# Optimization experiments

Hardware: AMD Instinct MI355X
Metric: run time of the kernel (lower is better)

Reference implementation:

```python
import jax, jax.numpy as jnp
import numpy as np

B, N, I, O, R = 8, 1024, 256, 256, 8


def setup_inputs() -> dict:
    key = jax.random.key(0)
    k1, k2, k3 = jax.random.split(key, 3)
    x = jax.random.normal(k1, (B, N, I), dtype=jnp.float32)
    adj = jax.random.uniform(k2, (B, N, N, R), dtype=jnp.float32)  # soft adjacency [b, src, dst, r]
    weight = jax.random.normal(k3, (R, I, O), dtype=jnp.float32)   # per-relation transform
    return {"x": x, "adj": adj, "weight": weight}


def reference(x, adj, weight):
    # per-relation transformed features: [b, src, r, o]
    f = jnp.einsum('bni,rio->bnro', x, weight)
    # contraction over source nodes and relations, weighted by soft adjacency:
    # out[b, dst, o] = sum_{src, r} adj[b, src, dst, r] * f[b, src, r, o]
    out = jnp.einsum('bnro,bnmr->bmo', f, adj)
    # normalization: total incoming soft-edge weight per destination node
    denom = jnp.clip(adj.sum(axis=(1, 3)), 1e-16, None)  # [b, dst]
    return out / denom[..., None]
```

## Files before the change

### kernel.cpp

```cpp
#include <hip/hip_runtime.h>
#include <stdint.h>


typedef float          floatx4  __attribute__((ext_vector_type(4)));
typedef short          shortx8  __attribute__((ext_vector_type(8)));
typedef unsigned short ushortx4 __attribute__((ext_vector_type(4)));
typedef unsigned short ushortx8 __attribute__((ext_vector_type(8)));

__device__ __forceinline__ unsigned short f2bf(float f) {
  union { float f; unsigned int u; } v; v.f = f;
  unsigned int u = v.u + 0x7FFFu + ((v.u >> 16) & 1u);
  return (unsigned short)(u >> 16);
}

__device__ __forceinline__ void gload16(const void* g, void* l) {
  __builtin_amdgcn_global_load_lds((__attribute__((address_space(1))) void*)g,
                                   (__attribute__((address_space(3))) void*)l,
                                   16, 0, 0);
}

__global__ __launch_bounds__(256) void prep_xw(const float* __restrict__ x,
                                               const float* __restrict__ w,
                                               unsigned short* __restrict__ xbf,
                                               unsigned short* __restrict__ wt) {
  int bid = blockIdx.x;
  if (bid < 1024) {
    int t = bid * 256 + threadIdx.x;
    const float4* p = (const float4*)x + (size_t)t * 2;
    float4 a = p[0], b4 = p[1];
    ushortx8 o;
    o[0] = f2bf(a.x);  o[1] = f2bf(a.y);  o[2] = f2bf(a.z);  o[3] = f2bf(a.w);
    o[4] = f2bf(b4.x); o[5] = f2bf(b4.y); o[6] = f2bf(b4.z); o[7] = f2bf(b4.w);
    *(ushortx8*)(xbf + (size_t)t * 8) = o;
  } else {
    int id = (bid - 1024) * 256 + threadIdx.x;
    int r = id >> 16, i = (id >> 8) & 255, o = id & 255;
    float v = w[((size_t)(r * 256 + i) << 8) + o];
    wt[((size_t)(o * 8 + r) << 8) + i] = f2bf(v);
  }
}

__global__ __launch_bounds__(256) void k1_gemm(const unsigned short* __restrict__ xbf,
                                               const unsigned short* __restrict__ wt,
                                               unsigned short* __restrict__ ft) {
  int bid = blockIdx.x;
  int m0 = (bid >> 4) * 128, n0 = (bid & 15) * 128;
  int l = threadIdx.x & 63, w = threadIdx.x >> 6;
  int lr = l & 15, lg = l >> 4;
  int mw = m0 + (w >> 1) * 64, nw = n0 + (w & 1) * 64;

  floatx4 acc[4][4] = {};
#pragma unroll
  for (int ks = 0; ks < 8; ++ks) {
    shortx8 a[4], b[4];
#pragma unroll
    for (int mi = 0; mi < 4; ++mi)
      a[mi] = *(const shortx8*)(xbf + (size_t)(mw + mi * 16 + lr) * 256 + ks * 32 + lg * 8);
#pragma unroll
    for (int ni = 0; ni < 4; ++ni)
      b[ni] = *(const shortx8*)(wt + (size_t)(nw + ni * 16 + lr) * 256 + ks * 32 + lg * 8);
#pragma unroll
    for (int mi = 0; mi < 4; ++mi)
#pragma unroll
      for (int ni = 0; ni < 4; ++ni)
        acc[mi][ni] = __builtin_amdgcn_mfma_f32_16x16x32_bf16(a[mi], b[ni], acc[mi][ni], 0, 0, 0);
  }
#pragma unroll
  for (int mi = 0; mi < 4; ++mi) {
#pragma unroll
    for (int ni = 0; ni < 4; ++ni) {
      int np = nw + ni * 16 + lr;
      int o = np >> 3, r = np & 7;
#pragma unroll
      for (int reg = 0; reg < 4; ++reg) {
        int row = mw + mi * 16 + lg * 4 + reg;
        int b8 = row >> 10, src = row & 1023;
        ft[((size_t)(b8 * 256 + o) << 13) + src * 8 + r] = f2bf(acc[mi][ni][reg]);
      }
    }
  }
}

#define BHALF 16384
#define AHALF 4096
__global__ __launch_bounds__(512) void k2_gemm(const float* __restrict__ adj,
                                               const unsigned short* __restrict__ ft,
                                               float* __restrict__ pout,
                                               float* __restrict__ dpart) {
  __shared__ __align__(16) unsigned short Blds[2 * BHALF];
  __shared__ __align__(16) unsigned short Alds[2 * AHALF];
  __shared__ float dsums[512];
  __shared__ float denr[64];

  int bid = blockIdx.x;
  int kc = bid >> 7;
  int inner = bid & 127;
  int b = inner & 7;
  int dst0 = (inner >> 3) * 64;

  int t = threadIdx.x, l = t & 63, w = t >> 6;
  int lr = l & 15, lg = l >> 4;
  int wm = w >> 2, wo = w & 3;

  int dst_l = (t >> 1) & 63;
  int rh = (t & 1) * 4;
  int sA = t >> 7;

  int csw = (l & 7) ^ (l >> 3);

  const size_t adj_b = (size_t)b << 23;
  const unsigned short* ftb = ft + ((size_t)b << 21);
  int src_base = kc * 512;
  const int KT = 64;

  float dsum = 0.f;
  floatx4 acc[2][4] = {};
  float4 av[2];

  auto A_load = [&](int kt, float4* v) {
#pragma unroll
    for (int j = 0; j < 2; ++j) {
      int src_l = sA + j * 4;
      v[j] = *(const float4*)(adj + adj_b + ((size_t)(src_base + kt * 8 + src_l) << 13)
                              + ((size_t)(dst0 + dst_l) << 3) + rh);
    }
  };
  auto A_store = [&](int half, const float4* v) {
#pragma unroll
    for (int j = 0; j < 2; ++j) {
      int src_l = sA + j * 4;
      float4 q = v[j];
      dsum += q.x + q.y + q.z + q.w;
      ushortx4 h;
      h[0] = f2bf(q.x); h[1] = f2bf(q.y); h[2] = f2bf(q.z); h[3] = f2bf(q.w);
      int slot = src_l ^ (dst_l & 7);
      *(ushortx4*)&Alds[half * AHALF + dst_l * 64 + slot * 8 + rh] = h;
    }
  };
  auto B_stage = [&](int kt, int half) {
    int kbase = (src_base + kt * 8) * 8;
#pragma unroll
    for (int i = 0; i < 4; ++i) {
      int orow = i * 64 + w * 8 + (l >> 3);
      const unsigned short* g = ftb + ((size_t)orow << 13) + kbase + (csw << 3);
      gload16(g, &Blds[half * BHALF + (i * 64 + w * 8) * 64]);
    }
  };
  auto compute = [&](int half) {
#pragma unroll
    for (int s = 0; s < 2; ++s) {
      int slotbase = s * 4 + lg;
      shortx8 af[2], bfr[4];
#pragma unroll
      for (int mi = 0; mi < 2; ++mi) {
        int row = wm * 32 + mi * 16 + lr;
        af[mi] = *(const shortx8*)&Alds[half * AHALF + row * 64 + ((slotbase ^ (row & 7)) << 3)];
      }
#pragma unroll
      for (int ni = 0; ni < 4; ++ni) {
        int oc = wo * 64 + ni * 16 + lr;
        bfr[ni] = *(const shortx8*)&Blds[half * BHALF + oc * 64 + ((slotbase ^ (oc & 7)) << 3)];
      }
#pragma unroll
      for (int mi = 0; mi < 2; ++mi)
#pragma unroll
        for (int ni = 0; ni < 4; ++ni)
          acc[mi][ni] = __builtin_amdgcn_mfma_f32_16x16x32_bf16(af[mi], bfr[ni], acc[mi][ni], 0, 0, 0);
    }
  };

  A_load(0, av);
  B_stage(0, 0);
  A_store(0, av);
  __syncthreads();

  for (int kt = 0; kt < KT; ++kt) {
    int cur = kt & 1, nxt = cur ^ 1;
    bool has = (kt + 1) < KT;
    if (has) A_load(kt + 1, av);
    if (has) B_stage(kt + 1, nxt);
    compute(cur);
    if (has) A_store(nxt, av);
    __syncthreads();
  }

  dsums[t] = dsum;
  __syncthreads();
  if (t < 64) {
    float s = 0.f;
#pragma unroll
    for (int sh = 0; sh < 4; ++sh) {
      s += dsums[sh * 128 + t * 2];
      s += dsums[sh * 128 + t * 2 + 1];
    }
    denr[t] = s;
  }
  __syncthreads();

#pragma unroll
  for (int mi = 0; mi < 2; ++mi) {
#pragma unroll
    for (int reg = 0; reg < 4; ++reg) {
      int row = dst0 + wm * 32 + mi * 16 + lg * 4 + reg;
#pragma unroll
      for (int ni = 0; ni < 4; ++ni) {
        int col = wo * 64 + ni * 16 + lr;
        pout[(size_t)kc * 2097152 + (((size_t)b << 10) + row) * 256 + col] = acc[mi][ni][reg];
      }
    }
  }
  if (t < 64) dpart[kc * 8192 + (b << 10) + dst0 + t] = denr[t];
}

__global__ __launch_bounds__(256) void k3_reduce(const float* __restrict__ pout,
                                                 const float* __restrict__ dpart,
                                                 float* __restrict__ outp) {
  int bid = blockIdx.x;
  size_t base = (size_t)bid * 256 + threadIdx.x;
  float v = pout[base] + pout[2097152 + base];
  float d = dpart[bid] + dpart[8192 + bid];
  outp[base] = v / fmaxf(d, 1e-16f);
}

extern "C" void kernel_launch(void* const* d_in, const int* in_sizes, int n_in,
                              void* d_out, int out_size, void* d_ws, size_t ws_size,
                              hipStream_t stream) {
  const float* x   = (const float*)d_in[0];
  const float* adj = (const float*)d_in[1];
  const float* w   = (const float*)d_in[2];
  float* out = (float*)d_out;

  char* ws = (char*)d_ws;
  unsigned short* ft  = (unsigned short*)(ws);
  unsigned short* xbf = (unsigned short*)(ws + 33554432);
  unsigned short* wt  = (unsigned short*)(ws + 37748736);
  float* pout  = (float*)(ws + 38797312);
  float* dpart = (float*)(ws + 55574528);

  prep_xw<<<3072, 256, 0, stream>>>(x, w, xbf, wt);
  k1_gemm<<<1024, 256, 0, stream>>>(xbf, wt, ft);
  k2_gemm<<<256, 512, 0, stream>>>(adj, ft, pout, dpart);
  k3_reduce<<<8192, 256, 0, stream>>>(pout, dpart, out);
}
```

Measured before the change: 149.8 us.

## Drop split-K reduction, triple-buffer k2 pipeline, vectorize k1 stores

k2_gemm now covers the full source dimension per block, with 32 destination rows instead of 64. This removes the partial-output workspace and the separate k3 reduce kernel, and normalization happens in the epilogue. The main loop uses a three-stage LDS ring, with manual vmcnt waits and raw s_barrier, so loads stay two tiles ahead. k1_gemm swaps its operand roles so each lane writes four contiguous bf16 relation values as one 8-byte store. The risks are halved MFMA work per A fragment and a longer serial K loop per block at the same grid size of 256.

```diff
diff --git a/kernel.cpp b/kernel.cpp
--- a/kernel.cpp
+++ b/kernel.cpp
@@ -18,6 +18,9 @@
                                    (__attribute__((address_space(3))) void*)l,
                                    16, 0, 0);
 }
+
+#define WAIT_V5 asm volatile("s_waitcnt vmcnt(5) lgkmcnt(0)" ::: "memory")
+#define WAIT_V0 asm volatile("s_waitcnt vmcnt(0) lgkmcnt(0)" ::: "memory")
 
 __global__ __launch_bounds__(256) void prep_xw(const float* __restrict__ x,
                                                const float* __restrict__ w,
@@ -44,182 +47,158 @@
                                                const unsigned short* __restrict__ wt,
                                                unsigned short* __restrict__ ft) {
   int bid = blockIdx.x;
-  int m0 = (bid >> 4) * 128, n0 = (bid & 15) * 128;
+  int p0 = (bid & 15) * 128, q0 = (bid >> 4) * 128;
   int l = threadIdx.x & 63, w = threadIdx.x >> 6;
   int lr = l & 15, lg = l >> 4;
-  int mw = m0 + (w >> 1) * 64, nw = n0 + (w & 1) * 64;
+  int pw = p0 + (w >> 1) * 64, qw = q0 + (w & 1) * 64;
 
   floatx4 acc[4][4] = {};
 #pragma unroll
   for (int ks = 0; ks < 8; ++ks) {
     shortx8 a[4], b[4];
 #pragma unroll
-    for (int mi = 0; mi < 4; ++mi)
-      a[mi] = *(const shortx8*)(xbf + (size_t)(mw + mi * 16 + lr) * 256 + ks * 32 + lg * 8);
-#pragma unroll
-    for (int ni = 0; ni < 4; ++ni)
-      b[ni] = *(const shortx8*)(wt + (size_t)(nw + ni * 16 + lr) * 256 + ks * 32 + lg * 8);
-#pragma unroll
-    for (int mi = 0; mi < 4; ++mi)
-#pragma unroll
-      for (int ni = 0; ni < 4; ++ni)
-        acc[mi][ni] = __builtin_amdgcn_mfma_f32_16x16x32_bf16(a[mi], b[ni], acc[mi][ni], 0, 0, 0);
-  }
-#pragma unroll
-  for (int mi = 0; mi < 4; ++mi) {
-#pragma unroll
-    for (int ni = 0; ni < 4; ++ni) {
-      int np = nw + ni * 16 + lr;
-      int o = np >> 3, r = np & 7;
-#pragma unroll
-      for (int reg = 0; reg < 4; ++reg) {
-        int row = mw + mi * 16 + lg * 4 + reg;
-        int b8 = row >> 10, src = row & 1023;
-        ft[((size_t)(b8 * 256 + o) << 13) + src * 8 + r] = f2bf(acc[mi][ni][reg]);
-      }
-    }
-  }
-}
-
-#define BHALF 16384
-#define AHALF 4096
+    for (int pi = 0; pi < 4; ++pi)
+      a[pi] = *(const shortx8*)(wt + (size_t)(pw + pi * 16 + lr) * 256 + ks * 32 + lg * 8);
+#pragma unroll
+    for (int qi = 0; qi < 4; ++qi)
+      b[qi] = *(const shortx8*)(xbf + (size_t)(qw + qi * 16 + lr) * 256 + ks * 32 + lg * 8);
+#pragma unroll
+    for (int pi = 0; pi < 4; ++pi)
+#pragma unroll
+      for (int qi = 0; qi < 4; ++qi)
+        acc[pi][qi] = __builtin_amdgcn_mfma_f32_16x16x32_bf16(a[pi], b[qi], acc[pi][qi], 0, 0, 0);
+  }
+#pragma unroll
+  for (int pi = 0; pi < 4; ++pi) {
+    int nbase = pw + pi * 16 + lg * 4;
+    int o = nbase >> 3, rb = nbase & 7;
+#pragma unroll
+    for (int qi = 0; qi < 4; ++qi) {
+      int m = qw + qi * 16 + lr;
+      int b8 = m >> 10, src = m & 1023;
+      ushortx4 h;
+      h[0] = f2bf(acc[pi][qi][0]); h[1] = f2bf(acc[pi][qi][1]);
+      h[2] = f2bf(acc[pi][qi][2]); h[3] = f2bf(acc[pi][qi][3]);
+      *(ushortx4*)(ft + ((size_t)(b8 * 256 + o) << 13) + src * 8 + rb) = h;
+    }
+  }
+}
+
+#define NKT 128
+#define BSZ (256 * 64)
+#define ASZ (32 * 64)
 __global__ __launch_bounds__(512) void k2_gemm(const float* __restrict__ adj,
                                                const unsigned short* __restrict__ ft,
-                                               float* __restrict__ pout,
-                                               float* __restrict__ dpart) {
-  __shared__ __align__(16) unsigned short Blds[2 * BHALF];
-  __shared__ __align__(16) unsigned short Alds[2 * AHALF];
+                                               float* __restrict__ outp) {
+  __shared__ __align__(16) unsigned short Blds[3 * BSZ];
+  __shared__ __align__(16) unsigned short Alds[3 * ASZ];
   __shared__ float dsums[512];
-  __shared__ float denr[64];
+  __shared__ float denr[32];
 
   int bid = blockIdx.x;
-  int kc = bid >> 7;
-  int inner = bid & 127;
-  int b = inner & 7;
-  int dst0 = (inner >> 3) * 64;
+  int b = bid & 7;
+  int dst0 = (bid >> 3) * 32;
 
   int t = threadIdx.x, l = t & 63, w = t >> 6;
   int lr = l & 15, lg = l >> 4;
   int wm = w >> 2, wo = w & 3;
 
-  int dst_l = (t >> 1) & 63;
+  int dst_l = (t >> 1) & 31;
   int rh = (t & 1) * 4;
-  int sA = t >> 7;
-
   int csw = (l & 7) ^ (l >> 3);
 
   const size_t adj_b = (size_t)b << 23;
   const unsigned short* ftb = ft + ((size_t)b << 21);
-  int src_base = kc * 512;
-  const int KT = 64;
 
   float dsum = 0.f;
-  floatx4 acc[2][4] = {};
-  float4 av[2];
-
-  auto A_load = [&](int kt, float4* v) {
-#pragma unroll
-    for (int j = 0; j < 2; ++j) {
-      int src_l = sA + j * 4;
-      v[j] = *(const float4*)(adj + adj_b + ((size_t)(src_base + kt * 8 + src_l) << 13)
-                              + ((size_t)(dst0 + dst_l) << 3) + rh);
-    }
-  };
-  auto A_store = [&](int half, const float4* v) {
-#pragma unroll
-    for (int j = 0; j < 2; ++j) {
-      int src_l = sA + j * 4;
-      float4 q = v[j];
-      dsum += q.x + q.y + q.z + q.w;
-      ushortx4 h;
-      h[0] = f2bf(q.x); h[1] = f2bf(q.y); h[2] = f2bf(q.z); h[3] = f2bf(q.w);
-      int slot = src_l ^ (dst_l & 7);
-      *(ushortx4*)&Alds[half * AHALF + dst_l * 64 + slot * 8 + rh] = h;
-    }
-  };
-  auto B_stage = [&](int kt, int half) {
-    int kbase = (src_base + kt * 8) * 8;
+  floatx4 acc[4] = {};
+  float4 av1, av2;
+
+  auto A_load = [&](int kt) -> float4 {
+    return *(const float4*)(adj + adj_b + ((size_t)(kt * 8 + w) << 13)
+                            + ((size_t)(dst0 + dst_l) << 3) + rh);
+  };
+  auto A_store = [&](float4 q, int buf) {
+    dsum += q.x + q.y + q.z + q.w;
+    ushortx4 h;
+    h[0] = f2bf(q.x); h[1] = f2bf(q.y); h[2] = f2bf(q.z); h[3] = f2bf(q.w);
+    int slot = w ^ (dst_l & 7);
+    *(ushortx4*)&Alds[buf * ASZ + dst_l * 64 + slot * 8 + rh] = h;
+  };
+  auto B_stage = [&](int kt, int buf) {
+    int kbase = kt * 64;
 #pragma unroll
     for (int i = 0; i < 4; ++i) {
       int orow = i * 64 + w * 8 + (l >> 3);
       const unsigned short* g = ftb + ((size_t)orow << 13) + kbase + (csw << 3);
-      gload16(g, &Blds[half * BHALF + (i * 64 + w * 8) * 64]);
-    }
-  };
-  auto compute = [&](int half) {
+      gload16(g, &Blds[buf * BSZ + (i * 64 + w * 8) * 64]);
+    }
+  };
+  auto compute = [&](int buf) {
 #pragma unroll
     for (int s = 0; s < 2; ++s) {
       int slotbase = s * 4 + lg;
-      shortx8 af[2], bfr[4];
-#pragma unroll
-      for (int mi = 0; mi < 2; ++mi) {
-        int row = wm * 32 + mi * 16 + lr;
-        af[mi] = *(const shortx8*)&Alds[half * AHALF + row * 64 + ((slotbase ^ (row & 7)) << 3)];
-      }
+      int arow = wm * 16 + lr;
+      shortx8 af = *(const shortx8*)&Alds[buf * ASZ + arow * 64 + ((slotbase ^ (arow & 7)) << 3)];
+      shortx8 bfr[4];
 #pragma unroll
       for (int ni = 0; ni < 4; ++ni) {
         int oc = wo * 64 + ni * 16 + lr;
-        bfr[ni] = *(const shortx8*)&Blds[half * BHALF + oc * 64 + ((slotbase ^ (oc & 7)) << 3)];
+        bfr[ni] = *(const shortx8*)&Blds[buf * BSZ + oc * 64 + ((slotbase ^ (oc & 7)) << 3)];
       }
 #pragma unroll
-      for (int mi = 0; mi < 2; ++mi)
-#pragma unroll
-        for (int ni = 0; ni < 4; ++ni)
-          acc[mi][ni] = __builtin_amdgcn_mfma_f32_16x16x32_bf16(af[mi], bfr[ni], acc[mi][ni], 0, 0, 0);
-    }
-  };
-
-  A_load(0, av);
+      for (int ni = 0; ni < 4; ++ni)
+        acc[ni] = __builtin_amdgcn_mfma_f32_16x16x32_bf16(af, bfr[ni], acc[ni], 0, 0, 0);
+    }
+  };
+
+  av1 = A_load(0);
   B_stage(0, 0);
-  A_store(0, av);
-  __syncthreads();
-
-  for (int kt = 0; kt < KT; ++kt) {
-    int cur = kt & 1, nxt = cur ^ 1;
-    bool has = (kt + 1) < KT;
-    if (has) A_load(kt + 1, av);
-    if (has) B_stage(kt + 1, nxt);
-    compute(cur);
-    if (has) A_store(nxt, av);
-    __syncthreads();
+  A_store(av1, 0);
+  av1 = A_load(1);
+  B_stage(1, 1);
+  WAIT_V5;
+  __builtin_amdgcn_s_barrier();
+
+  int c0 = 0, c1 = 1, c2 = 2;
+  for (int kt = 0; kt < NKT; ++kt) {
+    bool iss = (kt + 2) < NKT;
+    bool st  = (kt + 1) < NKT;
+    if (iss) { av2 = A_load(kt + 2); B_stage(kt + 2, c2); }
+    if (st)  { A_store(av1, c1); }
+    compute(c0);
+    if (st) {
+      if (iss) { WAIT_V5; } else { WAIT_V0; }
+      __builtin_amdgcn_s_barrier();
+    }
+    av1 = av2;
+    int tmp = c0; c0 = c1; c1 = c2; c2 = tmp;
   }
 
   dsums[t] = dsum;
   __syncthreads();
-  if (t < 64) {
+  if (t < 32) {
     float s = 0.f;
 #pragma unroll
-    for (int sh = 0; sh < 4; ++sh) {
-      s += dsums[sh * 128 + t * 2];
-      s += dsums[sh * 128 + t * 2 + 1];
+    for (int sl = 0; sl < 8; ++sl) {
+      s += dsums[sl * 64 + t * 2];
+      s += dsums[sl * 64 + t * 2 + 1];
     }
     denr[t] = s;
   }
   __syncthreads();
 
 #pragma unroll
-  for (int mi = 0; mi < 2; ++mi) {
-#pragma unroll
-    for (int reg = 0; reg < 4; ++reg) {
-      int row = dst0 + wm * 32 + mi * 16 + lg * 4 + reg;
-#pragma unroll
-      for (int ni = 0; ni < 4; ++ni) {
-        int col = wo * 64 + ni * 16 + lr;
-        pout[(size_t)kc * 2097152 + (((size_t)b << 10) + row) * 256 + col] = acc[mi][ni][reg];
-      }
-    }
-  }
-  if (t < 64) dpart[kc * 8192 + (b << 10) + dst0 + t] = denr[t];
-}
-
-__global__ __launch_bounds__(256) void k3_reduce(const float* __restrict__ pout,
-                                                 const float* __restrict__ dpart,
-                                                 float* __restrict__ outp) {
-  int bid = blockIdx.x;
-  size_t base = (size_t)bid * 256 + threadIdx.x;
-  float v = pout[base] + pout[2097152 + base];
-  float d = dpart[bid] + dpart[8192 + bid];
-  outp[base] = v / fmaxf(d, 1e-16f);
+  for (int reg = 0; reg < 4; ++reg) {
+    int rowl = wm * 16 + lg * 4 + reg;
+    float dinv = 1.f / fmaxf(denr[rowl], 1e-16f);
+    int row = dst0 + rowl;
+#pragma unroll
+    for (int ni = 0; ni < 4; ++ni) {
+      int col = wo * 64 + ni * 16 + lr;
+      outp[(((size_t)b << 10) + row) * 256 + col] = acc[ni][reg] * dinv;
+    }
+  }
 }
 
 extern "C" void kernel_launch(void* const* d_in, const int* in_sizes, int n_in,
@@ -234,11 +213,8 @@
   unsigned short* ft  = (unsigned short*)(ws);
   unsigned short* xbf = (unsigned short*)(ws + 33554432);
   unsigned short* wt  = (unsigned short*)(ws + 37748736);
-  float* pout  = (float*)(ws + 38797312);
-  float* dpart = (float*)(ws + 55574528);
 
   prep_xw<<<3072, 256, 0, stream>>>(x, w, xbf, wt);
   k1_gemm<<<1024, 256, 0, stream>>>(xbf, wt, ft);
-  k2_gemm<<<256, 512, 0, stream>>>(adj, ft, pout, dpart);
-  k3_reduce<<<8192, 256, 0, stream>>>(pout, dpart, out);
-}
+  k2_gemm<<<256, 512, 0, stream>>>(adj, ft, out);
+}
```

Result: slower. 175.4 us (+17.1%).

## Shrink k2 tiles to 32 dst rows with 256 threads; transpose k1 for vector stores

Applied to the files above, without the earlier changes.

k2 now uses 256-thread blocks, each covering 32 destination rows instead of 64, with twice as many blocks and launch bounds allowing two blocks per CU. This is meant to improve occupancy and spread the work across more CUs. The cost is that each B tile of ft is staged from global memory twice as often per destination. k1 swaps its operand roles so each lane holds four consecutive relation values and can write ft with packed 4-element bf16 stores instead of scalar scattered stores.

```diff
diff --git a/kernel.cpp b/kernel.cpp
--- a/kernel.cpp
+++ b/kernel.cpp
@@ -44,68 +44,62 @@
                                                const unsigned short* __restrict__ wt,
                                                unsigned short* __restrict__ ft) {
   int bid = blockIdx.x;
-  int m0 = (bid >> 4) * 128, n0 = (bid & 15) * 128;
+  int p0 = (bid & 15) * 128, q0 = (bid >> 4) * 128;
   int l = threadIdx.x & 63, w = threadIdx.x >> 6;
   int lr = l & 15, lg = l >> 4;
-  int mw = m0 + (w >> 1) * 64, nw = n0 + (w & 1) * 64;
+  int pw = p0 + (w >> 1) * 64, qw = q0 + (w & 1) * 64;
 
   floatx4 acc[4][4] = {};
 #pragma unroll
   for (int ks = 0; ks < 8; ++ks) {
     shortx8 a[4], b[4];
 #pragma unroll
-    for (int mi = 0; mi < 4; ++mi)
-      a[mi] = *(const shortx8*)(xbf + (size_t)(mw + mi * 16 + lr) * 256 + ks * 32 + lg * 8);
-#pragma unroll
-    for (int ni = 0; ni < 4; ++ni)
-      b[ni] = *(const shortx8*)(wt + (size_t)(nw + ni * 16 + lr) * 256 + ks * 32 + lg * 8);
-#pragma unroll
-    for (int mi = 0; mi < 4; ++mi)
-#pragma unroll
-      for (int ni = 0; ni < 4; ++ni)
-        acc[mi][ni] = __builtin_amdgcn_mfma_f32_16x16x32_bf16(a[mi], b[ni], acc[mi][ni], 0, 0, 0);
-  }
-#pragma unroll
-  for (int mi = 0; mi < 4; ++mi) {
-#pragma unroll
-    for (int ni = 0; ni < 4; ++ni) {
-      int np = nw + ni * 16 + lr;
-      int o = np >> 3, r = np & 7;
-#pragma unroll
-      for (int reg = 0; reg < 4; ++reg) {
-        int row = mw + mi * 16 + lg * 4 + reg;
-        int b8 = row >> 10, src = row & 1023;
-        ft[((size_t)(b8 * 256 + o) << 13) + src * 8 + r] = f2bf(acc[mi][ni][reg]);
-      }
-    }
-  }
-}
-
-#define BHALF 16384
-#define AHALF 4096
-__global__ __launch_bounds__(512) void k2_gemm(const float* __restrict__ adj,
-                                               const unsigned short* __restrict__ ft,
-                                               float* __restrict__ pout,
-                                               float* __restrict__ dpart) {
-  __shared__ __align__(16) unsigned short Blds[2 * BHALF];
-  __shared__ __align__(16) unsigned short Alds[2 * AHALF];
-  __shared__ float dsums[512];
-  __shared__ float denr[64];
-
-  int bid = blockIdx.x;
-  int kc = bid >> 7;
-  int inner = bid & 127;
-  int b = inner & 7;
-  int dst0 = (inner >> 3) * 64;
+    for (int pi = 0; pi < 4; ++pi)
+      a[pi] = *(const shortx8*)(wt + (size_t)(pw + pi * 16 + lr) * 256 + ks * 32 + lg * 8);
+#pragma unroll
+    for (int qi = 0; qi < 4; ++qi)
+      b[qi] = *(const shortx8*)(xbf + (size_t)(qw + qi * 16 + lr) * 256 + ks * 32 + lg * 8);
+#pragma unroll
+    for (int pi = 0; pi < 4; ++pi)
+#pragma unroll
+      for (int qi = 0; qi < 4; ++qi)
+        acc[pi][qi] = __builtin_amdgcn_mfma_f32_16x16x32_bf16(a[pi], b[qi], acc[pi][qi], 0, 0, 0);
+  }
+#pragma unroll
+  for (int pi = 0; pi < 4; ++pi) {
+    int nbase = pw + pi * 16 + lg * 4;
+    int o = nbase >> 3, rb = nbase & 7;
+#pragma unroll
+    for (int qi = 0; qi < 4; ++qi) {
+      int m = qw + qi * 16 + lr;
+      int b8 = m >> 10, src = m & 1023;
+      ushortx4 h;
+      h[0] = f2bf(acc[pi][qi][0]); h[1] = f2bf(acc[pi][qi][1]);
+      h[2] = f2bf(acc[pi][qi][2]); h[3] = f2bf(acc[pi][qi][3]);
+      *(ushortx4*)(ft + ((size_t)(b8 * 256 + o) << 13) + src * 8 + rb) = h;
+    }
+  }
+}
+
+#define BSZ (256 * 64)
+#define ASZ (32 * 64)
+__global__ __launch_bounds__(256, 2) void k2_gemm(const float* __restrict__ adj,
+                                                  const unsigned short* __restrict__ ft,
+                                                  float* __restrict__ pout,
+                                                  float* __restrict__ dpart) {
+  __shared__ __align__(16) unsigned short Blds[2 * BSZ];
+  __shared__ __align__(16) unsigned short Alds[2 * ASZ];
+
+  int bid = blockIdx.x;
+  int b = bid & 7;
+  int kc = (bid >> 3) & 1;
+  int dst0 = (bid >> 4) * 32;
 
   int t = threadIdx.x, l = t & 63, w = t >> 6;
   int lr = l & 15, lg = l >> 4;
-  int wm = w >> 2, wo = w & 3;
-
-  int dst_l = (t >> 1) & 63;
-  int rh = (t & 1) * 4;
-  int sA = t >> 7;
-
+
+  int dst_l = l >> 1;
+  int rh = (l & 1) * 4;
   int csw = (l & 7) ^ (l >> 3);
 
   const size_t adj_b = (size_t)b << 23;
@@ -120,46 +114,46 @@
   auto A_load = [&](int kt, float4* v) {
 #pragma unroll
     for (int j = 0; j < 2; ++j) {
-      int src_l = sA + j * 4;
+      int src_l = w + j * 4;
       v[j] = *(const float4*)(adj + adj_b + ((size_t)(src_base + kt * 8 + src_l) << 13)
                               + ((size_t)(dst0 + dst_l) << 3) + rh);
     }
   };
-  auto A_store = [&](int half, const float4* v) {
+  auto A_store = [&](int buf, const float4* v) {
 #pragma unroll
     for (int j = 0; j < 2; ++j) {
-      int src_l = sA + j * 4;
+      int src_l = w + j * 4;
       float4 q = v[j];
       dsum += q.x + q.y + q.z + q.w;
       ushortx4 h;
       h[0] = f2bf(q.x); h[1] = f2bf(q.y); h[2] = f2bf(q.z); h[3] = f2bf(q.w);
       int slot = src_l ^ (dst_l & 7);
-      *(ushortx4*)&Alds[half * AHALF + dst_l * 64 + slot * 8 + rh] = h;
-    }
-  };
-  auto B_stage = [&](int kt, int half) {
+      *(ushortx4*)&Alds[buf * ASZ + dst_l * 64 + slot * 8 + rh] = h;
+    }
+  };
+  auto B_stage = [&](int kt, int buf) {
     int kbase = (src_base + kt * 8) * 8;
 #pragma unroll
-    for (int i = 0; i < 4; ++i) {
-      int orow = i * 64 + w * 8 + (l >> 3);
+    for (int i = 0; i < 8; ++i) {
+      int orow = i * 32 + w * 8 + (l >> 3);
       const unsigned short* g = ftb + ((size_t)orow << 13) + kbase + (csw << 3);
-      gload16(g, &Blds[half * BHALF + (i * 64 + w * 8) * 64]);
-    }
-  };
-  auto compute = [&](int half) {
+      gload16(g, &Blds[buf * BSZ + (i * 32 + w * 8) * 64]);
+    }
+  };
+  auto compute = [&](int buf) {
 #pragma unroll
     for (int s = 0; s < 2; ++s) {
       int slotbase = s * 4 + lg;
       shortx8 af[2], bfr[4];
 #pragma unroll
       for (int mi = 0; mi < 2; ++mi) {
-        int row = wm * 32 + mi * 16 + lr;
-        af[mi] = *(const shortx8*)&Alds[half * AHALF + row * 64 + ((slotbase ^ (row & 7)) << 3)];
+        int arow = mi * 16 + lr;
+        af[mi] = *(const shortx8*)&Alds[buf * ASZ + arow * 64 + ((slotbase ^ (arow & 7)) << 3)];
       }
 #pragma unroll
       for (int ni = 0; ni < 4; ++ni) {
-        int oc = wo * 64 + ni * 16 + lr;
-        bfr[ni] = *(const shortx8*)&Blds[half * BHALF + oc * 64 + ((slotbase ^ (oc & 7)) << 3)];
+        int oc = w * 64 + ni * 16 + lr;
+        bfr[ni] = *(const shortx8*)&Blds[buf * BSZ + oc * 64 + ((slotbase ^ (oc & 7)) << 3)];
       }
 #pragma unroll
       for (int mi = 0; mi < 2; ++mi)
@@ -177,23 +171,24 @@
   for (int kt = 0; kt < KT; ++kt) {
     int cur = kt & 1, nxt = cur ^ 1;
     bool has = (kt + 1) < KT;
-    if (has) A_load(kt + 1, av);
-    if (has) B_stage(kt + 1, nxt);
+    if (has) { A_load(kt + 1, av); B_stage(kt + 1, nxt); }
     compute(cur);
     if (has) A_store(nxt, av);
     __syncthreads();
   }
 
-  dsums[t] = dsum;
+  float* dsf = (float*)Alds;
+  dsf[t] = dsum;
   __syncthreads();
-  if (t < 64) {
+  if (t < 32) {
     float s = 0.f;
 #pragma unroll
-    for (int sh = 0; sh < 4; ++sh) {
-      s += dsums[sh * 128 + t * 2];
-      s += dsums[sh * 128 + t * 2 + 1];
-    }
-    denr[t] = s;
+    for (int sl = 0; sl < 4; ++sl) {
+      s += dsf[sl * 64 + t * 2];
+      s += dsf[sl * 64 + t * 2 + 1];
+    }
+    dsf[256 + t] = s;
+    dpart[kc * 8192 + (b << 10) + dst0 + t] = s;
   }
   __syncthreads();
 
@@ -201,15 +196,14 @@
   for (int mi = 0; mi < 2; ++mi) {
 #pragma unroll
     for (int reg = 0; reg < 4; ++reg) {
-      int row = dst0 + wm * 32 + mi * 16 + lg * 4 + reg;
+      int row = dst0 + mi * 16 + lg * 4 + reg;
 #pragma unroll
       for (int ni = 0; ni < 4; ++ni) {
-        int col = wo * 64 + ni * 16 + lr;
+        int col = w * 64 + ni * 16 + lr;
         pout[(size_t)kc * 2097152 + (((size_t)b << 10) + row) * 256 + col] = acc[mi][ni][reg];
       }
     }
   }
-  if (t < 64) dpart[kc * 8192 + (b << 10) + dst0 + t] = denr[t];
 }
 
 __global__ __launch_bounds__(256) void k3_reduce(const float* __restrict__ pout,
@@ -239,6 +233,6 @@
 
   prep_xw<<<3072, 256, 0, stream>>>(x, w, xbf, wt);
   k1_gemm<<<1024, 256, 0, stream>>>(xbf, wt, ft);
-  k2_gemm<<<256, 512, 0, stream>>>(adj, ft, pout, dpart);
+  k2_gemm<<<512, 256, 0, stream>>>(adj, ft, pout, dpart);
   k3_reduce<<<8192, 256, 0, stream>>>(pout, dpart, out);
 }
```

Result: slower. 161.7 us (+7.9%).
